# Kernel optimization log

Hardware: AMD Instinct MI355X
Metric: run time of the kernel (lower is better)

Reference implementation:

```python
import jax, jax.numpy as jnp
import numpy as np

T, D, H, E = 8192, 1024, 2048, 8


def setup_inputs() -> dict:
    key = jax.random.key(0)
    k1, k2, k3 = jax.random.split(key, 3)
    x = jax.random.normal(k1, (T, D), dtype=jnp.float32)
    # counts must sum to T; use a uniform split (reference handles any valid split)
    num_tokens_per_expert = jnp.full((E,), T // E, dtype=jnp.int32)
    w_up = jax.random.normal(k2, (E, H, D), dtype=jnp.float32) * (1.0 / np.sqrt(D))
    w_down = jax.random.normal(k3, (E, D, H), dtype=jnp.float32) * (1.0 / np.sqrt(H))
    return {"x": x, "num_tokens_per_expert": num_tokens_per_expert, "w_up": w_up, "w_down": w_down}


def reference(x, num_tokens_per_expert, w_up, w_down):
    """Grouped MoE expert MLP: per-expert  x @ w_up[e].T -> relu^2 -> @ w_down[e].T.
    Tokens are sorted by expert; counts encode the segment boundaries.
    Matches the CUDA path: bf16 compute for both GEMMs and the activation,
    final cast back to x.dtype.
    """
    n_tok = x.shape[0]
    n_exp = w_up.shape[0]
    # segment id per token from cumulative offsets (same as grouped_mm offs)
    offsets = jnp.cumsum(num_tokens_per_expert)  # (E,)
    expert_id = jnp.searchsorted(offsets, jnp.arange(n_tok), side="right")  # (T,)

    xb = x.astype(jnp.bfloat16)
    wu = w_up.astype(jnp.bfloat16)   # (E, H, D)
    wd = w_down.astype(jnp.bfloat16)  # (E, D, H)

    out = jnp.zeros((n_tok, x.shape[1]), dtype=jnp.bfloat16)
    # small fixed loop over experts; token dim fully vectorized
    for e in range(n_exp):
        h = jnp.maximum(xb @ wu[e].T, 0)          # (T, H) relu
        h = (h * h).astype(jnp.bfloat16)           # square, re-cast as original
        y = h @ wd[e].T                            # (T, D)
        out = out + jnp.where((expert_id == e)[:, None], y, jnp.bfloat16(0))
    return out.astype(x.dtype)
```

## Files before the change

kernel.cpp:

```cpp
#include <hip/hip_runtime.h>
#include <stdint.h>

constexpr int T_TOK = 8192;
constexpr int D_DIM = 1024;
constexpr int H_DIM = 2048;
constexpr int E_NUM = 8;

typedef __bf16 bf16x8 __attribute__((ext_vector_type(8)));
typedef float  f32x4  __attribute__((ext_vector_type(4)));
typedef unsigned int u32x4 __attribute__((ext_vector_type(4)));

static __device__ __forceinline__ unsigned short f2bf(float f) {
  union { float f; unsigned u; } a; a.f = f;
  unsigned r = a.u + 0x7fffu + ((a.u >> 16) & 1u);
  return (unsigned short)(r >> 16);
}

__global__ void cvt_f32_bf16(const float* __restrict__ src,
                             unsigned short* __restrict__ dst, int n4) {
  int i = blockIdx.x * blockDim.x + threadIdx.x;
  int stride = gridDim.x * blockDim.x;
  for (; i < n4; i += stride) {
    float4 v = reinterpret_cast<const float4*>(src)[i];
    ushort4 o;
    o.x = f2bf(v.x); o.y = f2bf(v.y); o.z = f2bf(v.z); o.w = f2bf(v.w);
    reinterpret_cast<ushort4*>(dst)[i] = o;
  }
}

#define FENCE() asm volatile("" ::: "memory")
#define BARRIER() do { FENCE(); __builtin_amdgcn_s_barrier(); FENCE(); } while (0)
#define WAIT_LGKM0() asm volatile("s_waitcnt lgkmcnt(0)" ::: "memory")
#define WAIT_VM(N) asm volatile("s_waitcnt vmcnt(%0)" :: "i"(N) : "memory")
#define SCHED_FENCE() __builtin_amdgcn_sched_barrier(0)

static __device__ __forceinline__ f32x4 gload4(const void* p) {
  f32x4 r;
  asm volatile("global_load_dwordx4 %0, %1, off" : "=v"(r) : "v"(p) : "memory");
  return r;
}

template <int K_DIM, int N_DIM, int BN, bool RELU2>
__global__ __launch_bounds__(512, 2)
void gg8(const unsigned short* __restrict__ A,
         const float* __restrict__ Bw,
         const int* __restrict__ counts,
         void* __restrict__ Cout) {
  constexpr int BM = 256, BK = 64;
  constexpr int NT = K_DIM / BK;
  constexpr int WNC = BN / 4;
  constexpr int NACC = WNC / 16;
  constexpr int NQN = NACC / 2;
  constexpr int BL = (BN == 256) ? 4 : 2;
  constexpr int TSH = (BN == 256) ? 2 : 3;
  constexpr int FPB = BL * 16;

  const int tid  = threadIdx.x;
  const int wid  = tid >> 6;
  const int lane = tid & 63;
  const int wr   = wid >> 2;
  const int wc   = wid & 3;

  int t = blockIdx.x;
  int e = -1, rowBase = 0, rowsValid = 0;
  {
    int tiles = 0, off = 0;
#pragma unroll
    for (int i = 0; i < E_NUM; ++i) {
      int n  = counts[i];
      int nt = (n + BM - 1) / BM;
      if (e < 0 && t < tiles + nt) {
        e = i;
        int lt = t - tiles;
        rowBase   = off + lt * BM;
        rowsValid = n - lt * BM;
        if (rowsValid > BM) rowsValid = BM;
      }
      tiles += nt; off += n;
    }
  }
  if (e < 0) return;
  const int colBase = blockIdx.y * BN;

  __shared__ __align__(1024) char lds[(BM + BN) * BK * 2 * 2];
  auto ldsA = [&](int b) -> char* { return lds + b * (BM * 128); };
  auto ldsB = [&](int b) -> char* { return lds + 2 * (BM * 128) + b * (BN * 128); };

  const char* gA = (const char*)A + (size_t)rowBase * (K_DIM * 2);
  const int  bRow0 = tid >> TSH;
  const int  bByte = (tid & ((1 << TSH) - 1)) * FPB;
  const char* gBbase = (const char*)Bw +
      ((size_t)e * N_DIM + colBase) * (size_t)(K_DIM * 4);

  const int lr8 = lane >> 3;
  const int gsw = (lane & 7) ^ lr8;

  auto stageA = [&](int buf, int alpha, int kt) {
#pragma unroll
    for (int j = 0; j < 2; ++j) {
      int bi   = j * 8 + wid;
      int row0 = (bi >> 3) * 128 + alpha * 64 + (bi & 7) * 8;
      int sr   = row0 + lr8;
      if (sr >= rowsValid) sr = rowsValid - 1;
      const char* src = gA + (size_t)sr * (K_DIM * 2) + (size_t)kt * 128 + gsw * 16;
      __builtin_amdgcn_global_load_lds(
          (const __attribute__((address_space(1))) void*)src,
          (__attribute__((address_space(3))) void*)(ldsA(buf) + row0 * 128),
          16, 0, 0);
    }
  };

  auto loadBhalf = [&](f32x4 (&q)[BL], int h, int kt) {
    const char* s = gBbase + (size_t)(h * (BN / 2) + bRow0) * (K_DIM * 4)
                  + (size_t)kt * 256 + bByte;
#pragma unroll
    for (int j = 0; j < BL; ++j) q[j] = gload4(s + j * 16);
  };
  auto writeBhalf = [&](int buf, const f32x4 (&q)[BL], int h) {
    const int row = h * (BN / 2) + bRow0;
    char* base = ldsB(buf) + row * 128;
    const int rs = row & 7;
#pragma unroll
    for (int c = 0; c < BL / 2; ++c) {
      union { __bf16 b[8]; u32x4 w; } u;
#pragma unroll
      for (int k = 0; k < 2; ++k)
#pragma unroll
        for (int p = 0; p < 4; ++p)
          u.b[k * 4 + p] = (__bf16)q[c * 2 + k][p];
      int g = (BN == 256) ? (2 * (tid & 3) + c) : (tid & 7);
      *reinterpret_cast<u32x4*>(base + (g ^ rs) * 16) = u.w;
    }
  };

  const int rowLane = lane & 15;
  const int grpA    = lane >> 4;
  const int swzm    = lane & 7;

  bf16x8 aF[4][2];
  f32x4  accC[8][NACC];
#pragma unroll
  for (int m = 0; m < 8; ++m)
#pragma unroll
    for (int n = 0; n < NACC; ++n) accC[m][n] = (f32x4){0.f, 0.f, 0.f, 0.f};

  auto readA = [&](int buf, int rh) {
    const char* base = ldsA(buf) + (wr * 128 + rh * 64 + rowLane) * 128;
#pragma unroll
    for (int m = 0; m < 4; ++m)
#pragma unroll
      for (int ks = 0; ks < 2; ++ks) {
        int g = (ks * 4 + grpA) ^ swzm;
        aF[m][ks] = *(const bf16x8*)(base + m * (16 * 128) + g * 16);
      }
  };

  f32x4 bq0[BL], bq1[BL];

  loadBhalf(bq0, 0, 0);
  loadBhalf(bq1, 1, 0);
  stageA(0, 0, 0); stageA(0, 1, 0);
  WAIT_VM(BL + 4); SCHED_FENCE();
  writeBhalf(0, bq0, 0);
  loadBhalf(bq0, 0, 1);
  WAIT_VM(BL + 4); SCHED_FENCE();
  writeBhalf(0, bq1, 1);
  loadBhalf(bq1, 1, 1);
  WAIT_VM(2 * BL);
  WAIT_LGKM0();
  BARRIER();

  if constexpr (BN == 256) {
    bf16x8 bF0[NQN][2], bF1[NQN][2];
    auto readB = [&](int buf, int ch, bf16x8 (&dst)[NQN][2]) {
      const char* base = ldsB(buf) + (wc * WNC + ch * (WNC / 2) + rowLane) * 128;
#pragma unroll
      for (int n = 0; n < NQN; ++n)
#pragma unroll
        for (int ks = 0; ks < 2; ++ks) {
          int g = (ks * 4 + grpA) ^ swzm;
          dst[n][ks] = *(const bf16x8*)(base + n * (16 * 128) + g * 16);
        }
    };
#define MFMAQ(RH, CH, BFA)                                                    \
  do {                                                                        \
    __builtin_amdgcn_s_setprio(1);                                            \
    _Pragma("unroll")                                                         \
    for (int m_ = 0; m_ < 4; ++m_) {                                          \
      _Pragma("unroll")                                                       \
      for (int n_ = 0; n_ < NQN; ++n_) {                                      \
        f32x4 c_ = accC[(RH) * 4 + m_][(CH) * NQN + n_];                      \
        c_ = __builtin_amdgcn_mfma_f32_16x16x32_bf16(aF[m_][0], BFA[n_][0], c_, 0, 0, 0); \
        c_ = __builtin_amdgcn_mfma_f32_16x16x32_bf16(aF[m_][1], BFA[n_][1], c_, 0, 0, 0); \
        accC[(RH) * 4 + m_][(CH) * NQN + n_] = c_;                            \
      }                                                                       \
    }                                                                         \
    __builtin_amdgcn_s_setprio(0);                                            \
  } while (0)
    for (int t2 = 0; t2 < NT; ++t2) {
      const int cur = t2 & 1, nxt = cur ^ 1;
      const int ktn  = (t2 + 1 < NT) ? t2 + 1 : NT - 1;
      const int ktn2 = (t2 + 2 < NT) ? t2 + 2 : NT - 1;

      stageA(nxt, 0, ktn);
      stageA(nxt, 1, ktn);
      readA(cur, 0); readB(cur, 0, bF0);
      BARRIER(); WAIT_LGKM0();
      MFMAQ(0, 0, bF0);
      BARRIER();
      readB(cur, 1, bF1);
      BARRIER(); WAIT_LGKM0();
      MFMAQ(0, 1, bF1);
      BARRIER();
      WAIT_VM(BL + 4);
      SCHED_FENCE();
      writeBhalf(nxt, bq0, 0);
      loadBhalf(bq0, 0, ktn2);
      readA(cur, 1);
      BARRIER(); WAIT_LGKM0();
      MFMAQ(1, 1, bF1);
      BARRIER();
      WAIT_VM(BL + 4);
      SCHED_FENCE();
      writeBhalf(nxt, bq1, 1);
      loadBhalf(bq1, 1, ktn2);
      WAIT_VM(2 * BL);
      BARRIER(); WAIT_LGKM0();
      MFMAQ(1, 0, bF0);
      BARRIER();
    }
#undef MFMAQ
  } else {
    bf16x8 bFall[NACC][2];
    auto readBall = [&](int buf) {
      const char* base = ldsB(buf) + (wc * WNC + rowLane) * 128;
#pragma unroll
      for (int n = 0; n < NACC; ++n)
#pragma unroll
        for (int ks = 0; ks < 2; ++ks) {
          int g = (ks * 4 + grpA) ^ swzm;
          bFall[n][ks] = *(const bf16x8*)(base + n * (16 * 128) + g * 16);
        }
    };
#define MFMAQ2(RH)                                                            \
  do {                                                                        \
    __builtin_amdgcn_s_setprio(1);                                            \
    _Pragma("unroll")                                                         \
    for (int m_ = 0; m_ < 4; ++m_) {                                          \
      _Pragma("unroll")                                                       \
      for (int n_ = 0; n_ < NACC; ++n_) {                                     \
        f32x4 c_ = accC[(RH) * 4 + m_][n_];                                   \
        c_ = __builtin_amdgcn_mfma_f32_16x16x32_bf16(aF[m_][0], bFall[n_][0], c_, 0, 0, 0); \
        c_ = __builtin_amdgcn_mfma_f32_16x16x32_bf16(aF[m_][1], bFall[n_][1], c_, 0, 0, 0); \
        accC[(RH) * 4 + m_][n_] = c_;                                         \
      }                                                                       \
    }                                                                         \
    __builtin_amdgcn_s_setprio(0);                                            \
  } while (0)
    for (int t2 = 0; t2 < NT; ++t2) {
      const int cur = t2 & 1, nxt = cur ^ 1;
      const int ktn  = (t2 + 1 < NT) ? t2 + 1 : NT - 1;
      const int ktn2 = (t2 + 2 < NT) ? t2 + 2 : NT - 1;

      stageA(nxt, 0, ktn);
      stageA(nxt, 1, ktn);
      WAIT_VM(6);
      SCHED_FENCE();
      writeBhalf(nxt, bq0, 0);
      loadBhalf(bq0, 0, ktn2);
      readA(cur, 0); readBall(cur);
      BARRIER(); WAIT_LGKM0();
      MFMAQ2(0);
      BARRIER();
      WAIT_VM(6);
      SCHED_FENCE();
      writeBhalf(nxt, bq1, 1);
      loadBhalf(bq1, 1, ktn2);
      readA(cur, 1);
      WAIT_VM(4);
      BARRIER(); WAIT_LGKM0();
      MFMAQ2(1);
      BARRIER();
    }
#undef MFMAQ2
  }

  WAIT_VM(0);
  SCHED_FENCE();
#pragma unroll
  for (int j = 0; j < BL; ++j) {
    asm volatile("" :: "v"(bq0[j]), "v"(bq1[j]));
  }

  const int rB0 = wr * 128 + grpA * 4;
  const int cB0 = colBase + wc * WNC + rowLane;
#pragma unroll
  for (int m = 0; m < 8; ++m) {
#pragma unroll
    for (int n = 0; n < NACC; ++n) {
#pragma unroll
      for (int j = 0; j < 4; ++j) {
        int r = rB0 + m * 16 + j;
        if (r < rowsValid) {
          size_t idx = (size_t)(rowBase + r) * N_DIM + (cB0 + n * 16);
          float v = accC[m][n][j];
          if (RELU2) {
            float rl = v > 0.f ? v : 0.f;
            float hf = (float)(__bf16)rl;
            ((__bf16*)Cout)[idx] = (__bf16)(hf * hf);
          } else {
            ((float*)Cout)[idx] = (float)(__bf16)v;
          }
        }
      }
    }
  }
}

extern "C" void kernel_launch(void* const* d_in, const int* in_sizes, int n_in,
                              void* d_out, int out_size, void* d_ws, size_t ws_size,
                              hipStream_t stream) {
  const float* x   = (const float*)d_in[0];
  const int*   cnt = (const int*)d_in[1];
  const float* wu  = (const float*)d_in[2];
  const float* wd  = (const float*)d_in[3];
  float* out = (float*)d_out;
  char*  ws  = (char*)d_ws;

  unsigned short* xb   = (unsigned short*)(ws);
  unsigned short* hbuf = (unsigned short*)(ws + (16u << 20));

  cvt_f32_bf16<<<2048, 256, 0, stream>>>(x, xb, T_TOK * D_DIM / 4);

  gg8<D_DIM, H_DIM, 256, true ><<<dim3(40, H_DIM / 256), dim3(512), 0, stream>>>(
      xb, wu, cnt, (void*)hbuf);
  gg8<H_DIM, D_DIM, 128, false><<<dim3(40, D_DIM / 128), dim3(512), 0, stream>>>(
      hbuf, wd, cnt, (void*)out);
}
```

Before: 113.7 us.

## Overlap w_down bf16 conversion with first GEMM and use async LDS loads in second GEMM

The first GEMM kernel gets extra blocks that convert w_down from fp32 to bf16 into workspace, running alongside the up-projection tiles. The down-projection kernel then reads pre-converted bf16 weights through direct global-to-LDS loads, with no in-register conversion. This removes the per-tile fp32 weight loads and conversion from the second GEMM's inner loop. In exchange the conversion blocks compete for bandwidth and compute slots with the first GEMM, and 32MB of extra workspace traffic is added.

```diff
diff --git a/kernel.cpp b/kernel.cpp
--- a/kernel.cpp
+++ b/kernel.cpp
@@ -5,6 +5,7 @@
 constexpr int D_DIM = 1024;
 constexpr int H_DIM = 2048;
 constexpr int E_NUM = 8;
+constexpr int CVX   = 27;
 
 typedef __bf16 bf16x8 __attribute__((ext_vector_type(8)));
 typedef float  f32x4  __attribute__((ext_vector_type(4)));
@@ -40,22 +41,33 @@
   return r;
 }
 
-template <int K_DIM, int N_DIM, int BN, bool RELU2>
 __global__ __launch_bounds__(512, 2)
-void gg8(const unsigned short* __restrict__ A,
+void gg1(const unsigned short* __restrict__ A,
          const float* __restrict__ Bw,
          const int* __restrict__ counts,
-         void* __restrict__ Cout) {
-  constexpr int BM = 256, BK = 64;
+         unsigned short* __restrict__ Hout,
+         const float* __restrict__ cvsrc,
+         unsigned short* __restrict__ cvdst) {
+  constexpr int K_DIM = D_DIM, N_DIM = H_DIM;
+  constexpr int BM = 256, BK = 64, BN = 256;
   constexpr int NT = K_DIM / BK;
-  constexpr int WNC = BN / 4;
-  constexpr int NACC = WNC / 16;
-  constexpr int NQN = NACC / 2;
-  constexpr int BL = (BN == 256) ? 4 : 2;
-  constexpr int TSH = (BN == 256) ? 2 : 3;
-  constexpr int FPB = BL * 16;
-
-  const int tid  = threadIdx.x;
+  constexpr int WNC = 64, NACC = 4, NQN = 2, BL = 4, TSH = 2, FPB = 64;
+
+  const int tid = threadIdx.x;
+
+  if (blockIdx.x >= 40) {
+    const int cid = (blockIdx.x - 40) * 8 + blockIdx.y;
+    constexpr int CVN4  = E_NUM * D_DIM * H_DIM / 4;
+    constexpr int CVSTR = CVX * 8 * 512;
+    for (int i = cid * 512 + tid; i < CVN4; i += CVSTR) {
+      float4 v = reinterpret_cast<const float4*>(cvsrc)[i];
+      ushort4 o;
+      o.x = f2bf(v.x); o.y = f2bf(v.y); o.z = f2bf(v.z); o.w = f2bf(v.w);
+      reinterpret_cast<ushort4*>(cvdst)[i] = o;
+    }
+    return;
+  }
+
   const int wid  = tid >> 6;
   const int lane = tid & 63;
   const int wr   = wid >> 2;
@@ -128,7 +140,7 @@
 #pragma unroll
         for (int p = 0; p < 4; ++p)
           u.b[k * 4 + p] = (__bf16)q[c * 2 + k][p];
-      int g = (BN == 256) ? (2 * (tid & 3) + c) : (tid & 7);
+      int g = 2 * (tid & 3) + c;
       *reinterpret_cast<u32x4*>(base + (g ^ rs) * 16) = u.w;
     }
   };
@@ -154,34 +166,18 @@
         aF[m][ks] = *(const bf16x8*)(base + m * (16 * 128) + g * 16);
       }
   };
-
-  f32x4 bq0[BL], bq1[BL];
-
-  loadBhalf(bq0, 0, 0);
-  loadBhalf(bq1, 1, 0);
-  stageA(0, 0, 0); stageA(0, 1, 0);
-  WAIT_VM(BL + 4); SCHED_FENCE();
-  writeBhalf(0, bq0, 0);
-  loadBhalf(bq0, 0, 1);
-  WAIT_VM(BL + 4); SCHED_FENCE();
-  writeBhalf(0, bq1, 1);
-  loadBhalf(bq1, 1, 1);
-  WAIT_VM(2 * BL);
-  WAIT_LGKM0();
-  BARRIER();
-
-  if constexpr (BN == 256) {
-    bf16x8 bF0[NQN][2], bF1[NQN][2];
-    auto readB = [&](int buf, int ch, bf16x8 (&dst)[NQN][2]) {
-      const char* base = ldsB(buf) + (wc * WNC + ch * (WNC / 2) + rowLane) * 128;
-#pragma unroll
-      for (int n = 0; n < NQN; ++n)
-#pragma unroll
-        for (int ks = 0; ks < 2; ++ks) {
-          int g = (ks * 4 + grpA) ^ swzm;
-          dst[n][ks] = *(const bf16x8*)(base + n * (16 * 128) + g * 16);
-        }
-    };
+  bf16x8 bF0[NQN][2], bF1[NQN][2];
+  auto readB = [&](int buf, int ch, bf16x8 (&dst)[NQN][2]) {
+    const char* base = ldsB(buf) + (wc * WNC + ch * (WNC / 2) + rowLane) * 128;
+#pragma unroll
+    for (int n = 0; n < NQN; ++n)
+#pragma unroll
+      for (int ks = 0; ks < 2; ++ks) {
+        int g = (ks * 4 + grpA) ^ swzm;
+        dst[n][ks] = *(const bf16x8*)(base + n * (16 * 128) + g * 16);
+      }
+  };
+
 #define MFMAQ(RH, CH, BFA)                                                    \
   do {                                                                        \
     __builtin_amdgcn_s_setprio(1);                                            \
@@ -197,93 +193,55 @@
     }                                                                         \
     __builtin_amdgcn_s_setprio(0);                                            \
   } while (0)
-    for (int t2 = 0; t2 < NT; ++t2) {
-      const int cur = t2 & 1, nxt = cur ^ 1;
-      const int ktn  = (t2 + 1 < NT) ? t2 + 1 : NT - 1;
-      const int ktn2 = (t2 + 2 < NT) ? t2 + 2 : NT - 1;
-
-      stageA(nxt, 0, ktn);
-      stageA(nxt, 1, ktn);
-      readA(cur, 0); readB(cur, 0, bF0);
-      BARRIER(); WAIT_LGKM0();
-      MFMAQ(0, 0, bF0);
-      BARRIER();
-      readB(cur, 1, bF1);
-      BARRIER(); WAIT_LGKM0();
-      MFMAQ(0, 1, bF1);
-      BARRIER();
-      WAIT_VM(BL + 4);
-      SCHED_FENCE();
-      writeBhalf(nxt, bq0, 0);
-      loadBhalf(bq0, 0, ktn2);
-      readA(cur, 1);
-      BARRIER(); WAIT_LGKM0();
-      MFMAQ(1, 1, bF1);
-      BARRIER();
-      WAIT_VM(BL + 4);
-      SCHED_FENCE();
-      writeBhalf(nxt, bq1, 1);
-      loadBhalf(bq1, 1, ktn2);
-      WAIT_VM(2 * BL);
-      BARRIER(); WAIT_LGKM0();
-      MFMAQ(1, 0, bF0);
-      BARRIER();
-    }
+
+  f32x4 bq0[BL], bq1[BL];
+
+  loadBhalf(bq0, 0, 0);
+  loadBhalf(bq1, 1, 0);
+  stageA(0, 0, 0); stageA(0, 1, 0);
+  WAIT_VM(BL + 4); SCHED_FENCE();
+  writeBhalf(0, bq0, 0);
+  loadBhalf(bq0, 0, 1);
+  WAIT_VM(BL + 4); SCHED_FENCE();
+  writeBhalf(0, bq1, 1);
+  loadBhalf(bq1, 1, 1);
+  WAIT_VM(2 * BL);
+  WAIT_LGKM0();
+  BARRIER();
+
+  for (int t2 = 0; t2 < NT; ++t2) {
+    const int cur = t2 & 1, nxt = cur ^ 1;
+    const int ktn  = (t2 + 1 < NT) ? t2 + 1 : NT - 1;
+    const int ktn2 = (t2 + 2 < NT) ? t2 + 2 : NT - 1;
+
+    stageA(nxt, 0, ktn);
+    stageA(nxt, 1, ktn);
+    readA(cur, 0); readB(cur, 0, bF0);
+    BARRIER(); WAIT_LGKM0();
+    MFMAQ(0, 0, bF0);
+    BARRIER();
+    readB(cur, 1, bF1);
+    BARRIER(); WAIT_LGKM0();
+    MFMAQ(0, 1, bF1);
+    BARRIER();
+    WAIT_VM(BL + 4);
+    SCHED_FENCE();
+    writeBhalf(nxt, bq0, 0);
+    loadBhalf(bq0, 0, ktn2);
+    readA(cur, 1);
+    BARRIER(); WAIT_LGKM0();
+    MFMAQ(1, 1, bF1);
+    BARRIER();
+    WAIT_VM(BL + 4);
+    SCHED_FENCE();
+    writeBhalf(nxt, bq1, 1);
+    loadBhalf(bq1, 1, ktn2);
+    WAIT_VM(2 * BL);
+    BARRIER(); WAIT_LGKM0();
+    MFMAQ(1, 0, bF0);
+    BARRIER();
+  }
 #undef MFMAQ
-  } else {
-    bf16x8 bFall[NACC][2];
-    auto readBall = [&](int buf) {
-      const char* base = ldsB(buf) + (wc * WNC + rowLane) * 128;
-#pragma unroll
-      for (int n = 0; n < NACC; ++n)
-#pragma unroll
-        for (int ks = 0; ks < 2; ++ks) {
-          int g = (ks * 4 + grpA) ^ swzm;
-          bFall[n][ks] = *(const bf16x8*)(base + n * (16 * 128) + g * 16);
-        }
-    };
-#define MFMAQ2(RH)                                                            \
-  do {                                                                        \
-    __builtin_amdgcn_s_setprio(1);                                            \
-    _Pragma("unroll")                                                         \
-    for (int m_ = 0; m_ < 4; ++m_) {                                          \
-      _Pragma("unroll")                                                       \
-      for (int n_ = 0; n_ < NACC; ++n_) {                                     \
-        f32x4 c_ = accC[(RH) * 4 + m_][n_];                                   \
-        c_ = __builtin_amdgcn_mfma_f32_16x16x32_bf16(aF[m_][0], bFall[n_][0], c_, 0, 0, 0); \
-        c_ = __builtin_amdgcn_mfma_f32_16x16x32_bf16(aF[m_][1], bFall[n_][1], c_, 0, 0, 0); \
-        accC[(RH) * 4 + m_][n_] = c_;                                         \
-      }                                                                       \
-    }                                                                         \
-    __builtin_amdgcn_s_setprio(0);                                            \
-  } while (0)
-    for (int t2 = 0; t2 < NT; ++t2) {
-      const int cur = t2 & 1, nxt = cur ^ 1;
-      const int ktn  = (t2 + 1 < NT) ? t2 + 1 : NT - 1;
-      const int ktn2 = (t2 + 2 < NT) ? t2 + 2 : NT - 1;
-
-      stageA(nxt, 0, ktn);
-      stageA(nxt, 1, ktn);
-      WAIT_VM(6);
-      SCHED_FENCE();
-      writeBhalf(nxt, bq0, 0);
-      loadBhalf(bq0, 0, ktn2);
-      readA(cur, 0); readBall(cur);
-      BARRIER(); WAIT_LGKM0();
-      MFMAQ2(0);
-      BARRIER();
-      WAIT_VM(6);
-      SCHED_FENCE();
-      writeBhalf(nxt, bq1, 1);
-      loadBhalf(bq1, 1, ktn2);
-      readA(cur, 1);
-      WAIT_VM(4);
-      BARRIER(); WAIT_LGKM0();
-      MFMAQ2(1);
-      BARRIER();
-    }
-#undef MFMAQ2
-  }
 
   WAIT_VM(0);
   SCHED_FENCE();
@@ -304,13 +262,198 @@
         if (r < rowsValid) {
           size_t idx = (size_t)(rowBase + r) * N_DIM + (cB0 + n * 16);
           float v = accC[m][n][j];
-          if (RELU2) {
-            float rl = v > 0.f ? v : 0.f;
-            float hf = (float)(__bf16)rl;
-            ((__bf16*)Cout)[idx] = (__bf16)(hf * hf);
-          } else {
-            ((float*)Cout)[idx] = (float)(__bf16)v;
-          }
+          float rl = v > 0.f ? v : 0.f;
+          float hf = (float)(__bf16)rl;
+          ((__bf16*)Hout)[idx] = (__bf16)(hf * hf);
+        }
+      }
+    }
+  }
+}
+
+template <int K_DIM, int N_DIM>
+__global__ __launch_bounds__(512, 2)
+void gg2(const unsigned short* __restrict__ A,
+         const unsigned short* __restrict__ Bw,
+         const int* __restrict__ counts,
+         float* __restrict__ Cout) {
+  constexpr int BM = 256, BK = 64, BN = 128;
+  constexpr int NT = K_DIM / BK;
+  constexpr int NITER = NT / 2;
+  constexpr int WNC = 32, VN = 5;
+
+  const int tid  = threadIdx.x;
+  const int wid  = tid >> 6;
+  const int lane = tid & 63;
+  const int wr   = wid >> 2;
+  const int wc   = wid & 3;
+
+  int t = blockIdx.x;
+  int e = -1, rowBase = 0, rowsValid = 0;
+  {
+    int tiles = 0, off = 0;
+#pragma unroll
+    for (int i = 0; i < E_NUM; ++i) {
+      int n  = counts[i];
+      int nt = (n + BM - 1) / BM;
+      if (e < 0 && t < tiles + nt) {
+        e = i;
+        int lt = t - tiles;
+        rowBase   = off + lt * BM;
+        rowsValid = n - lt * BM;
+        if (rowsValid > BM) rowsValid = BM;
+      }
+      tiles += nt; off += n;
+    }
+  }
+  if (e < 0) return;
+  const int colBase = blockIdx.y * BN;
+
+  __shared__ __align__(1024) char lds[(BM + BN) * BK * 2 * 2];
+  auto ldsA = [&](int b) -> char* { return lds + b * (BM * 128); };
+  auto ldsB = [&](int b) -> char* { return lds + 2 * (BM * 128) + b * (BN * 128); };
+
+  const char* gA = (const char*)A + (size_t)rowBase * (K_DIM * 2);
+  const char* gB = (const char*)Bw + ((size_t)e * N_DIM + colBase) * (size_t)(K_DIM * 2);
+
+  const int lr8 = lane >> 3;
+  const int gsw = (lane & 7) ^ lr8;
+
+  auto stageA = [&](int buf, int alpha, int kt) {
+#pragma unroll
+    for (int j = 0; j < 2; ++j) {
+      int bi   = j * 8 + wid;
+      int row0 = (bi >> 3) * 128 + alpha * 64 + (bi & 7) * 8;
+      int sr   = row0 + lr8;
+      if (sr >= rowsValid) sr = rowsValid - 1;
+      const char* src = gA + (size_t)sr * (K_DIM * 2) + (size_t)kt * 128 + gsw * 16;
+      __builtin_amdgcn_global_load_lds(
+          (const __attribute__((address_space(1))) void*)src,
+          (__attribute__((address_space(3))) void*)(ldsA(buf) + row0 * 128),
+          16, 0, 0);
+    }
+  };
+  auto stageB = [&](int buf, int alpha, int kt) {
+    int bi   = wid;
+    int row0 = (bi >> 1) * 32 + alpha * 16 + (bi & 1) * 8;
+    int sr   = row0 + lr8;
+    const char* src = gB + (size_t)sr * (K_DIM * 2) + (size_t)kt * 128 + gsw * 16;
+    __builtin_amdgcn_global_load_lds(
+        (const __attribute__((address_space(1))) void*)src,
+        (__attribute__((address_space(3))) void*)(ldsB(buf) + row0 * 128),
+        16, 0, 0);
+  };
+
+  const int rowLane = lane & 15;
+  const int grpA    = lane >> 4;
+  const int swzm    = lane & 7;
+
+  bf16x8 aF[4][2];
+  bf16x8 bF0[2], bF1[2];
+  f32x4  accC[8][2];
+#pragma unroll
+  for (int m = 0; m < 8; ++m)
+#pragma unroll
+    for (int n = 0; n < 2; ++n) accC[m][n] = (f32x4){0.f, 0.f, 0.f, 0.f};
+
+  auto readA = [&](int buf, int rh) {
+    const char* base = ldsA(buf) + (wr * 128 + rh * 64 + rowLane) * 128;
+#pragma unroll
+    for (int m = 0; m < 4; ++m)
+#pragma unroll
+      for (int ks = 0; ks < 2; ++ks) {
+        int g = (ks * 4 + grpA) ^ swzm;
+        aF[m][ks] = *(const bf16x8*)(base + m * (16 * 128) + g * 16);
+      }
+  };
+  auto readB = [&](int buf, int ch, bf16x8 (&dst)[2]) {
+    const char* base = ldsB(buf) + (wc * WNC + ch * 16 + rowLane) * 128;
+#pragma unroll
+    for (int ks = 0; ks < 2; ++ks) {
+      int g = (ks * 4 + grpA) ^ swzm;
+      dst[ks] = *(const bf16x8*)(base + g * 16);
+    }
+  };
+
+#define MFMAQ2(RH, CH, BFA)                                                   \
+  do {                                                                        \
+    __builtin_amdgcn_s_setprio(1);                                            \
+    _Pragma("unroll")                                                         \
+    for (int m_ = 0; m_ < 4; ++m_) {                                          \
+      f32x4 c_ = accC[(RH) * 4 + m_][(CH)];                                   \
+      c_ = __builtin_amdgcn_mfma_f32_16x16x32_bf16(aF[m_][0], BFA[0], c_, 0, 0, 0); \
+      c_ = __builtin_amdgcn_mfma_f32_16x16x32_bf16(aF[m_][1], BFA[1], c_, 0, 0, 0); \
+      accC[(RH) * 4 + m_][(CH)] = c_;                                         \
+    }                                                                         \
+    __builtin_amdgcn_s_setprio(0);                                            \
+  } while (0)
+
+  stageA(0, 0, 0); stageB(0, 0, 0); stageA(0, 1, 0); stageB(0, 1, 0);
+  stageA(1, 0, 1); stageB(1, 0, 1); stageA(1, 1, 1);
+  WAIT_VM(VN);
+  BARRIER();
+
+  for (int it = 0; it < NITER; ++it) {
+    const int t0  = 2 * it;
+    const int kB1 = t0 + 1;
+    const int kN0 = (t0 + 2 < NT) ? t0 + 2 : NT - 1;
+    const int kN1 = (t0 + 3 < NT) ? t0 + 3 : NT - 1;
+
+    readA(0, 0); readB(0, 0, bF0);
+    stageB(1, 1, kB1);
+    BARRIER(); WAIT_LGKM0();
+    MFMAQ2(0, 0, bF0);
+    BARRIER();
+    readB(0, 1, bF1);
+    stageA(0, 0, kN0);
+    BARRIER(); WAIT_LGKM0();
+    MFMAQ2(0, 1, bF1);
+    BARRIER();
+    readA(0, 1);
+    stageB(0, 0, kN0);
+    BARRIER(); WAIT_LGKM0();
+    MFMAQ2(1, 1, bF1);
+    BARRIER();
+    stageA(0, 1, kN0);
+    WAIT_VM(VN);
+    BARRIER();
+    MFMAQ2(1, 0, bF0);
+    BARRIER();
+    readA(1, 0); readB(1, 0, bF0);
+    stageB(0, 1, kN0);
+    BARRIER(); WAIT_LGKM0();
+    MFMAQ2(0, 0, bF0);
+    BARRIER();
+    readB(1, 1, bF1);
+    stageA(1, 0, kN1);
+    BARRIER(); WAIT_LGKM0();
+    MFMAQ2(0, 1, bF1);
+    BARRIER();
+    readA(1, 1);
+    stageB(1, 0, kN1);
+    BARRIER(); WAIT_LGKM0();
+    MFMAQ2(1, 1, bF1);
+    BARRIER();
+    stageA(1, 1, kN1);
+    WAIT_VM(VN);
+    BARRIER();
+    MFMAQ2(1, 0, bF0);
+    BARRIER();
+  }
+#undef MFMAQ2
+
+  const int rB0 = wr * 128 + grpA * 4;
+  const int cB0 = colBase + wc * WNC + rowLane;
+#pragma unroll
+  for (int m = 0; m < 8; ++m) {
+#pragma unroll
+    for (int n = 0; n < 2; ++n) {
+#pragma unroll
+      for (int j = 0; j < 4; ++j) {
+        int r = rB0 + m * 16 + j;
+        if (r < rowsValid) {
+          size_t idx = (size_t)(rowBase + r) * N_DIM + (cB0 + n * 16);
+          Cout[idx] = (float)(__bf16)accC[m][n][j];
         }
       }
     }
@@ -329,11 +472,13 @@
 
   unsigned short* xb   = (unsigned short*)(ws);
   unsigned short* hbuf = (unsigned short*)(ws + (16u << 20));
+  unsigned short* wdb  = (unsigned short*)(ws + (48u << 20));
 
   cvt_f32_bf16<<<2048, 256, 0, stream>>>(x, xb, T_TOK * D_DIM / 4);
 
-  gg8<D_DIM, H_DIM, 256, true ><<<dim3(40, H_DIM / 256), dim3(512), 0, stream>>>(
-      xb, wu, cnt, (void*)hbuf);
-  gg8<H_DIM, D_DIM, 128, false><<<dim3(40, D_DIM / 128), dim3(512), 0, stream>>>(
-      hbuf, wd, cnt, (void*)out);
-}
+  gg1<<<dim3(40 + CVX, H_DIM / 256), dim3(512), 0, stream>>>(
+      xb, wu, cnt, hbuf, wd, wdb);
+
+  gg2<H_DIM, D_DIM><<<dim3(40, D_DIM / 128), dim3(512), 0, stream>>>(
+      hbuf, wdb, cnt, out);
+}
```

Measured after the change: 150.2 us. +32.1%, slower.
